# Kernel tuning notes

Hardware: AMD Instinct MI355X
Metric: run time of the kernel (lower is better)

The kernel has to match this reference:

```python
import jax, jax.numpy as jnp
import numpy as np

BATCH = 2048
NUM_CLASSES = 50000
FEAT_DIM = 256
CLAMP_MIN = 1e-12
CLAMP_MAX = 1e12


def setup_inputs() -> dict:
    key = jax.random.key(0)
    k1, k2, k3 = jax.random.split(key, 3)
    x = jax.random.normal(k1, (BATCH, FEAT_DIM), dtype=jnp.float32)
    labels = jax.random.randint(k2, (BATCH,), 0, NUM_CLASSES, dtype=jnp.int64)
    centers = jax.random.normal(k3, (NUM_CLASSES, FEAT_DIM), dtype=jnp.float32)
    return {"x": x, "labels": labels, "centers": centers}


def reference(x, labels, centers):
    # x: [B, D], centers: [C, D], labels: [B]
    batch_size = x.shape[0]
    num_classes = centers.shape[0]
    # Full pairwise squared-distance matrix [B, C] (as in the original module)
    distmat = (
        jnp.sum(x * x, axis=1, keepdims=True)              # [B, 1]
        + jnp.sum(centers * centers, axis=1)[None, :]      # [1, C]
        - 2.0 * jnp.einsum("bd,cd->bc", x, centers)       # [B, C]
    )
    # One-hot label mask, applied multiplicatively (zeros elsewhere)
    mask = (labels[:, None] == jnp.arange(num_classes)[None, :]).astype(distmat.dtype)
    dist = distmat * mask
    # NOTE: faithful to original — clamp is applied to ALL entries (masked zeros
    # become CLAMP_MIN), then summed.
    loss = jnp.sum(jnp.clip(dist, CLAMP_MIN, CLAMP_MAX)) / batch_size
    return loss
```

## Files before the change

### kernel.cpp

```cpp
#include <hip/hip_runtime.h>

#define BATCH 2048
#define NUM_CLASSES 50000
#define FEAT_DIM 256
#define CLAMP_MIN 1e-12f
#define CLAMP_MAX 1e12f

__global__ void __launch_bounds__(256)
row_dist_kernel(const float* __restrict__ x,
                const int* __restrict__ labels,
                const float* __restrict__ centers,
                float* __restrict__ row_out) {
    const int wave = threadIdx.x >> 6;
    const int lane = threadIdx.x & 63;
    const int b = (blockIdx.x << 2) + wave;

    const int lab = __builtin_amdgcn_readfirstlane(labels[b]);

    const float4 xv = *reinterpret_cast<const float4*>(
        x + (size_t)b * FEAT_DIM + lane * 4);
    const float4 cv = *reinterpret_cast<const float4*>(
        centers + (size_t)lab * FEAT_DIM + lane * 4);

    const float dx = xv.x - cv.x;
    const float dy = xv.y - cv.y;
    const float dz = xv.z - cv.z;
    const float dw = xv.w - cv.w;
    float s = dx * dx + dy * dy + dz * dz + dw * dw;

    #pragma unroll
    for (int off = 32; off > 0; off >>= 1)
        s += __shfl_down(s, off, 64);

    if (lane == 0) {
        s = fminf(fmaxf(s, CLAMP_MIN), CLAMP_MAX);
        row_out[b] = s;
    }
}

__global__ void __launch_bounds__(64)
final_reduce_kernel(const float* __restrict__ row_out, float* __restrict__ out) {
    const int lane = threadIdx.x;
    float s = 0.f;
    #pragma unroll
    for (int j = 0; j < 8; ++j) {
        const float4 v = *reinterpret_cast<const float4*>(
            row_out + j * 256 + lane * 4);
        s += v.x + v.y + v.z + v.w;
    }
    #pragma unroll
    for (int off = 32; off > 0; off >>= 1)
        s += __shfl_down(s, off, 64);

    if (lane == 0) {
        const double masked = (double)(NUM_CLASSES - 1) * 1e-12;
        out[0] = (float)((double)s / (double)BATCH + masked);
    }
}

extern "C" void kernel_launch(void* const* d_in, const int* in_sizes, int n_in,
                              void* d_out, int out_size, void* d_ws, size_t ws_size,
                              hipStream_t stream) {
    const float* x       = (const float*)d_in[0];
    const int*   labels  = (const int*)d_in[1];
    const float* centers = (const float*)d_in[2];
    float* out = (float*)d_out;
    float* ws  = (float*)d_ws;

    row_dist_kernel<<<BATCH / 4, 256, 0, stream>>>(x, labels, centers, ws);
    final_reduce_kernel<<<1, 64, 0, stream>>>(ws, out);
}
```

Baseline: 11.40 us.

## Fuse row distance and final reduction into one cooperative kernel with grid sync

Replaces the two-kernel pipeline with a single cooperative launch of 256 blocks. Each wave now handles two rows and each block writes one partial sum to workspace. After a grid-wide sync, block 0 reduces the 256 partials and writes the loss. This removes a second kernel launch and the gap between launches, at the cost of cooperative-launch overhead and a grid barrier.

```diff
diff --git a/kernel.cpp b/kernel.cpp
--- a/kernel.cpp
+++ b/kernel.cpp
@@ -1,60 +1,77 @@
 #include <hip/hip_runtime.h>
+#include <hip/hip_cooperative_groups.h>
+namespace cg = cooperative_groups;
 
 #define BATCH 2048
 #define NUM_CLASSES 50000
 #define FEAT_DIM 256
 #define CLAMP_MIN 1e-12f
 #define CLAMP_MAX 1e12f
+#define NBLK 256
+#define NTHR 256
 
-__global__ void __launch_bounds__(256)
-row_dist_kernel(const float* __restrict__ x,
-                const int* __restrict__ labels,
-                const float* __restrict__ centers,
-                float* __restrict__ row_out) {
+__global__ void __launch_bounds__(NTHR)
+fused_center_loss_kernel(const float* __restrict__ x,
+                         const int* __restrict__ labels,
+                         const float* __restrict__ centers,
+                         float* __restrict__ ws,
+                         float* __restrict__ out) {
+    __shared__ float sm[NTHR / 64];
     const int wave = threadIdx.x >> 6;
     const int lane = threadIdx.x & 63;
-    const int b = (blockIdx.x << 2) + wave;
+    const int w = (blockIdx.x << 2) + wave;
 
-    const int lab = __builtin_amdgcn_readfirstlane(labels[b]);
+    float s0 = 0.f, s1 = 0.f;
+    {
+        const int b0 = w;
+        const int b1 = w + 1024;
+        const int lab0 = __builtin_amdgcn_readfirstlane(labels[b0]);
+        const int lab1 = __builtin_amdgcn_readfirstlane(labels[b1]);
 
-    const float4 xv = *reinterpret_cast<const float4*>(
-        x + (size_t)b * FEAT_DIM + lane * 4);
-    const float4 cv = *reinterpret_cast<const float4*>(
-        centers + (size_t)lab * FEAT_DIM + lane * 4);
+        const float4 xv0 = *reinterpret_cast<const float4*>(
+            x + (size_t)b0 * FEAT_DIM + lane * 4);
+        const float4 cv0 = *reinterpret_cast<const float4*>(
+            centers + (size_t)lab0 * FEAT_DIM + lane * 4);
+        const float4 xv1 = *reinterpret_cast<const float4*>(
+            x + (size_t)b1 * FEAT_DIM + lane * 4);
+        const float4 cv1 = *reinterpret_cast<const float4*>(
+            centers + (size_t)lab1 * FEAT_DIM + lane * 4);
 
-    const float dx = xv.x - cv.x;
-    const float dy = xv.y - cv.y;
-    const float dz = xv.z - cv.z;
-    const float dw = xv.w - cv.w;
-    float s = dx * dx + dy * dy + dz * dz + dw * dw;
+        float dx = xv0.x - cv0.x, dy = xv0.y - cv0.y,
+              dz = xv0.z - cv0.z, dw = xv0.w - cv0.w;
+        s0 = dx * dx + dy * dy + dz * dz + dw * dw;
+        dx = xv1.x - cv1.x; dy = xv1.y - cv1.y;
+        dz = xv1.z - cv1.z; dw = xv1.w - cv1.w;
+        s1 = dx * dx + dy * dy + dz * dz + dw * dw;
+    }
 
     #pragma unroll
-    for (int off = 32; off > 0; off >>= 1)
-        s += __shfl_down(s, off, 64);
+    for (int off = 32; off > 0; off >>= 1) {
+        s0 += __shfl_down(s0, off, 64);
+        s1 += __shfl_down(s1, off, 64);
+    }
 
     if (lane == 0) {
-        s = fminf(fmaxf(s, CLAMP_MIN), CLAMP_MAX);
-        row_out[b] = s;
+        s0 = fminf(fmaxf(s0, CLAMP_MIN), CLAMP_MAX);
+        s1 = fminf(fmaxf(s1, CLAMP_MIN), CLAMP_MAX);
+        sm[wave] = s0 + s1;
     }
-}
+    __syncthreads();
+    if (threadIdx.x == 0)
+        ws[blockIdx.x] = sm[0] + sm[1] + sm[2] + sm[3];
 
-__global__ void __launch_bounds__(64)
-final_reduce_kernel(const float* __restrict__ row_out, float* __restrict__ out) {
-    const int lane = threadIdx.x;
-    float s = 0.f;
-    #pragma unroll
-    for (int j = 0; j < 8; ++j) {
-        const float4 v = *reinterpret_cast<const float4*>(
-            row_out + j * 256 + lane * 4);
-        s += v.x + v.y + v.z + v.w;
-    }
-    #pragma unroll
-    for (int off = 32; off > 0; off >>= 1)
-        s += __shfl_down(s, off, 64);
+    cg::this_grid().sync();
 
-    if (lane == 0) {
-        const double masked = (double)(NUM_CLASSES - 1) * 1e-12;
-        out[0] = (float)((double)s / (double)BATCH + masked);
+    if (blockIdx.x == 0 && threadIdx.x < 64) {
+        const float4 v = *reinterpret_cast<const float4*>(ws + lane * 4);
+        float s = v.x + v.y + v.z + v.w;
+        #pragma unroll
+        for (int off = 32; off > 0; off >>= 1)
+            s += __shfl_down(s, off, 64);
+        if (lane == 0) {
+            const double masked = (double)(NUM_CLASSES - 1) * 1e-12;
+            out[0] = (float)((double)s / (double)BATCH + masked);
+        }
     }
 }
 
@@ -67,6 +84,8 @@
     float* out = (float*)d_out;
     float* ws  = (float*)d_ws;
 
-    row_dist_kernel<<<BATCH / 4, 256, 0, stream>>>(x, labels, centers, ws);
-    final_reduce_kernel<<<1, 64, 0, stream>>>(ws, out);
+    void* args[] = {(void*)&x, (void*)&labels, (void*)&centers,
+                    (void*)&ws, (void*)&out};
+    hipLaunchCooperativeKernel((void*)fused_center_loss_kernel,
+                               dim3(NBLK), dim3(NTHR), args, 0, stream);
 }
```

New measurement: 42.81 us. +275.5%, slower.
